# Performance work log

Measured on AMD Instinct MI355X. Metric: run time of the kernel, lower is better.

The kernel has to match this reference:

```python
import jax, jax.numpy as jnp
import numpy as np

# dims
T, B, D = 128, 512, 512          # seq, batch, d_input = dim_aug_state*n_agent
M, H, DH, DFF = 6, 2, 32, 64     # mem_len, heads, d_head_inner, d_ff_inner
ACT = 64                          # dim_action*n_agent
BG = 0.1                          # GRU-gate bias (GTrXL)


def _ln(t, g, b):
    mu = t.mean(-1, keepdims=True)
    var = ((t - mu) ** 2).mean(-1, keepdims=True)
    return (t - mu) / jnp.sqrt(var + 1e-5) * g + b


def _rel_shift(x):
    # x: [T, J, B, H] -> TransformerXL relative shift
    Tq, J = x.shape[0], x.shape[1]
    zp = jnp.zeros((Tq, 1) + x.shape[2:], x.dtype)
    x = jnp.concatenate([zp, x], axis=1)              # [T, J+1, B, H]
    x = x.reshape((J + 1, Tq) + x.shape[2:])[1:]      # [J, T, B, H]
    return x.reshape((Tq, J) + x.shape[2:])


def _gate(x, y, W, b):
    # GRU-style gating g(x, y): x = residual stream, y = new branch output
    lin = lambda t, i: t @ W[i] + b[i]
    r = jax.nn.sigmoid(lin(y, 0) + lin(x, 1))
    z = jax.nn.sigmoid(lin(y, 2) + lin(x, 3) - BG)
    h = jnp.tanh(lin(y, 4) + (r * x) @ W[5] + b[5])
    return (1.0 - z) * x + z * h


def setup_inputs() -> dict:
    key = jax.random.key(0)
    ks = iter(jax.random.split(key, 32))
    rn = lambda shape, s=0.02: jax.random.normal(next(ks), shape, jnp.float32) * s
    return dict(
        aug_states=jax.random.normal(next(ks), (T, B, D), jnp.float32),
        action=jax.random.normal(next(ks), (B, ACT), jnp.float32),
        memory=jnp.zeros((M, B, D), jnp.float32),
        W_q=rn((D, H * DH)), W_kv=rn((D, 2 * H * DH)), W_p=rn((D, H * DH)), W_out=rn((H * DH, D)),
        u=rn((H, DH)), v=rn((H, DH)),
        ln1_g=jnp.ones(D), ln1_b=jnp.zeros(D), ln2_g=jnp.ones(D), ln2_b=jnp.zeros(D),
        ff_W1=rn((D, DFF)), ff_b1=jnp.zeros(DFF), ff_W2=rn((DFF, D)), ff_b2=jnp.zeros(D),
        g1_W=rn((6, D, D)), g1_b=jnp.zeros((6, D)), g2_W=rn((6, D, D)), g2_b=jnp.zeros((6, D)),
        d1_W=rn((D, 1024)), d1_b=jnp.zeros(1024),
        d2_W=rn((1024 + ACT, 512)), d2_b=jnp.zeros(512),
        d3_W=rn((512, 300)), d3_b=jnp.zeros(300),
        d4_W=rn((300, 1)), d4_b=jnp.zeros(1),
    )


def reference(aug_states, action, memory, W_q, W_kv, W_p, W_out, u, v,
              ln1_g, ln1_b, ln2_g, ln2_b, ff_W1, ff_b1, ff_W2, ff_b2,
              g1_W, g1_b, g2_W, g2_b, d1_W, d1_b, d2_W, d2_b, d3_W, d3_b, d4_W, d4_b):
    x = aug_states                                    # [T, B, D]
    J = T + M
    # sinusoidal relative position embeddings for positions J-1 .. 0
    pos = jnp.arange(J - 1, -1, -1.0, dtype=jnp.float32)
    inv_freq = 1.0 / (10000.0 ** (jnp.arange(0, D, 2, dtype=jnp.float32) / D))
    si = pos[:, None] * inv_freq[None, :]
    pos_emb = jnp.concatenate([jnp.sin(si), jnp.cos(si)], axis=-1)   # [J, D]

    # --- stable (pre-LN + gated) TransformerXL layer ---
    src2 = _ln(x, ln1_g, ln1_b)
    cat = jnp.concatenate([memory, src2], axis=0)     # [J, B, D]
    k, vv = jnp.split(cat @ W_kv, 2, axis=-1)
    q = (src2 @ W_q).reshape(T, B, H, DH)
    k = k.reshape(J, B, H, DH)
    vv = vv.reshape(J, B, H, DH)
    p = (pos_emb @ W_p).reshape(J, H, DH)
    content = jnp.einsum("ibhd,jbhd->ijbh", q + u, k)
    position = _rel_shift(jnp.einsum("ibhd,jhd->ijbh", q + v, p))
    attn = content + position                         # [T, J, B, H]
    mask = jnp.arange(J)[None, :] > (jnp.arange(T)[:, None] + M)     # causal w/ memory offset
    attn = jnp.where(mask[:, :, None, None], -jnp.inf, attn)
    attn = jax.nn.softmax(attn * (1.0 / np.sqrt(DH)), axis=1)
    av = jnp.einsum("ijbh,jbhd->ibhd", attn, vv).reshape(T, B, H * DH)
    src = _gate(x, av @ W_out, g1_W, g1_b)
    ff = jax.nn.relu(_ln(src, ln2_g, ln2_b) @ ff_W1 + ff_b1) @ ff_W2 + ff_b2
    out = _gate(src, ff, g2_W, g2_b)                  # [T, B, D]

    # --- mean pool + MLP critic head ---
    ts = out.mean(axis=0)                             # [B, D]
    h1 = jax.nn.relu(ts @ d1_W + d1_b)
    h = jnp.concatenate([h1, action], axis=1)
    h = jax.nn.relu(h @ d2_W + d2_b)
    h = jax.nn.relu(h @ d3_W + d3_b)
    return jax.nn.relu(h @ d4_W + d4_b)               # [B, 1]
```

## Files before the change

kernel.cpp:

```cpp
#include <hip/hip_runtime.h>
#include <math.h>

namespace {

constexpr int kT = 128, kB = 512, kD = 512, kM = 6, kH = 2;
constexpr int kJ = kT + kM;
constexpr float kBG = 0.1f;
constexpr int kTB = kT * kB;
constexpr int kBK = 32;

typedef __attribute__((ext_vector_type(8))) short bf16x8;
typedef __attribute__((ext_vector_type(4))) float f32x4;
typedef __attribute__((ext_vector_type(8))) unsigned short us8;
typedef __attribute__((ext_vector_type(4))) unsigned short us4;

__device__ __forceinline__ float sigmoidf_(float x) {
  return 1.0f / (1.0f + __expf(-x));
}

__device__ __forceinline__ unsigned short bf16u(float f) {
  union { float f; unsigned u; } c; c.f = f;
  unsigned r = c.u + 0x7fffu + ((c.u >> 16) & 1u);
  return (unsigned short)(r >> 16);
}

__device__ __forceinline__ float b2f(unsigned short u) {
  union { unsigned u; float f; } c; c.u = (unsigned)u << 16;
  return c.f;
}

__device__ __forceinline__ void gl_lds16(const void* g, void* l) {
  __builtin_amdgcn_global_load_lds(
      (const __attribute__((address_space(1))) unsigned int*)g,
      (__attribute__((address_space(3))) unsigned int*)l, 16, 0, 0);
}

template <int N>
__device__ __forceinline__ void wvm_() {
  asm volatile("s_waitcnt vmcnt(%0)" :: "n"(N) : "memory");
}
__device__ __forceinline__ void bar_() { __builtin_amdgcn_s_barrier(); }
__device__ __forceinline__ void cfence_() { asm volatile("" ::: "memory"); }


__global__ __launch_bounds__(256) void transp_kernel(const float* __restrict__ W,
                                                     unsigned short* __restrict__ Wt,
                                                     int K, int N) {
  __shared__ float t[32][33];
  const int n0 = blockIdx.x * 32, k0 = blockIdx.y * 32;
  const float* Wb = W + (size_t)blockIdx.z * K * N;
  unsigned short* Wtb = Wt + (size_t)blockIdx.z * K * N;
  int tx = threadIdx.x & 31, ty = threadIdx.x >> 5;
#pragma unroll
  for (int r = 0; r < 32; r += 8)
    t[ty + r][tx] = Wb[(size_t)(k0 + ty + r) * N + n0 + tx];
  __syncthreads();
#pragma unroll
  for (int r = 0; r < 32; r += 8)
    Wtb[(size_t)(n0 + ty + r) * K + k0 + tx] = bf16u(t[tx][ty + r]);
}

__global__ __launch_bounds__(256) void conv_bf16_kernel(const float* __restrict__ in,
                                                        unsigned short* __restrict__ outb,
                                                        size_t n) {
  size_t idx = ((size_t)blockIdx.x * 256 + threadIdx.x) * 8;
  if (idx >= n) return;
  float4 a = *(const float4*)(in + idx);
  float4 c = *(const float4*)(in + idx + 4);
  us8 o;
  o[0] = bf16u(a.x); o[1] = bf16u(a.y); o[2] = bf16u(a.z); o[3] = bf16u(a.w);
  o[4] = bf16u(c.x); o[5] = bf16u(c.y); o[6] = bf16u(c.z); o[7] = bf16u(c.w);
  *(us8*)(outb + idx) = o;
}

__global__ __launch_bounds__(256) void ln1_dual_kernel(const float* __restrict__ in,
                                                       const float* __restrict__ g,
                                                       const float* __restrict__ b,
                                                       unsigned short* __restrict__ outLN,
                                                       unsigned short* __restrict__ outRaw,
                                                       int nrows) {
  int wave = threadIdx.x >> 6, lane = threadIdx.x & 63;
  int row = blockIdx.x * 4 + wave;
  if (row >= nrows) return;
  const float* p = in + (size_t)row * kD + lane * 8;
  float4 a = *(const float4*)p;
  float4 c = *(const float4*)(p + 4);
  float v[8] = {a.x, a.y, a.z, a.w, c.x, c.y, c.z, c.w};
  float s = 0.f;
#pragma unroll
  for (int i = 0; i < 8; ++i) s += v[i];
#pragma unroll
  for (int off = 32; off; off >>= 1) s += __shfl_xor(s, off);
  float mu = s * (1.0f / 512.0f);
  float q = 0.f;
#pragma unroll
  for (int i = 0; i < 8; ++i) { float d = v[i] - mu; q += d * d; }
#pragma unroll
  for (int off = 32; off; off >>= 1) q += __shfl_xor(q, off);
  float rstd = rsqrtf(q * (1.0f / 512.0f) + 1e-5f);
  us8 oln, oraw;
#pragma unroll
  for (int i = 0; i < 8; ++i) {
    int col = lane * 8 + i;
    oln[i] = bf16u((v[i] - mu) * rstd * g[col] + b[col]);
    oraw[i] = bf16u(v[i]);
  }
  size_t off8 = (size_t)row * kD + lane * 8;
  *(us8*)(outLN + off8) = oln;
  *(us8*)(outRaw + off8) = oraw;
}

__global__ __launch_bounds__(256) void ln_b16_kernel(const unsigned short* __restrict__ in,
                                                     const float* __restrict__ g,
                                                     const float* __restrict__ b,
                                                     unsigned short* __restrict__ outb,
                                                     int nrows) {
  int wave = threadIdx.x >> 6, lane = threadIdx.x & 63;
  int row = blockIdx.x * 4 + wave;
  if (row >= nrows) return;
  us8 iv = *(const us8*)(in + (size_t)row * kD + lane * 8);
  float v[8];
#pragma unroll
  for (int i = 0; i < 8; ++i) v[i] = b2f(iv[i]);
  float s = 0.f;
#pragma unroll
  for (int i = 0; i < 8; ++i) s += v[i];
#pragma unroll
  for (int off = 32; off; off >>= 1) s += __shfl_xor(s, off);
  float mu = s * (1.0f / 512.0f);
  float q = 0.f;
#pragma unroll
  for (int i = 0; i < 8; ++i) { float d = v[i] - mu; q += d * d; }
#pragma unroll
  for (int off = 32; off; off >>= 1) q += __shfl_xor(q, off);
  float rstd = rsqrtf(q * (1.0f / 512.0f) + 1e-5f);
  us8 o;
#pragma unroll
  for (int i = 0; i < 8; ++i) {
    int col = lane * 8 + i;
    o[i] = bf16u((v[i] - mu) * rstd * g[col] + b[col]);
  }
  *(us8*)(outb + (size_t)row * kD + lane * 8) = o;
}

template <int TN, int EPI>
__global__ __launch_bounds__(256) void mfma_gemm_bt(
    const unsigned short* __restrict__ A, const unsigned short* __restrict__ Bt,
    int K, const float* __restrict__ bias, void* __restrict__ Cv, int N) {
  constexpr int MI = (TN == 128) ? 4 : 2;
  constexpr int NJ = 4;
  constexpr int BCH = TN * 64 / 1024;
  constexpr int NLD = 2 + BCH / 4;
  __shared__ __align__(16) unsigned short As[3][128 * kBK];
  __shared__ __align__(16) unsigned short Bs[3][TN * kBK];
  const int tid = threadIdx.x;
  const int lane = tid & 63, wv = tid >> 6;
  const int ml = lane & 15, qd = lane >> 4;
  const int swc = ((lane & 3) ^ ((lane >> 3) & 3)) * 16;
  const int qdx = qd ^ ((ml >> 1) & 3);
  const int m0 = blockIdx.y * 128, n0 = blockIdx.x * TN;
  const int mw0 = (TN == 128) ? (wv >> 1) * 64 : wv * 32;
  const int nw0 = (TN == 128) ? (wv & 1) * 64 : 0;
  const size_t ldA = (size_t)K * 2, ldB = (size_t)K * 2;
  const char* Ab = (const char*)A + (size_t)m0 * ldA;
  const char* Bb = (const char*)Bt + (size_t)n0 * ldB;
  auto stg = [&](int k0, int buf) {
#pragma unroll
    for (int c = wv; c < 8; c += 4) {
      int fb = c * 1024 + lane * 16;
      gl_lds16(Ab + (size_t)(fb >> 6) * ldA + swc + (size_t)k0 * 2,
               (char*)As[buf] + c * 1024 + lane * 16);
    }
#pragma unroll
    for (int c = wv; c < BCH; c += 4) {
      int fb = c * 1024 + lane * 16;
      gl_lds16(Bb + (size_t)(fb >> 6) * ldB + swc + (size_t)k0 * 2,
               (char*)Bs[buf] + c * 1024 + lane * 16);
    }
  };
  f32x4 acc[MI][NJ];
#pragma unroll
  for (int i = 0; i < MI; ++i)
#pragma unroll
    for (int j = 0; j < NJ; ++j) acc[i][j] = (f32x4)0.f;
  stg(0, 0);
  stg(kBK, 1);
  int cb = 0;
  for (int k0 = 0; k0 < K; k0 += kBK) {
    const int sb = (cb == 0) ? 2 : cb - 1;
    if (k0 + 2 * kBK < K) { stg(k0 + 2 * kBK, sb); wvm_<2 * NLD>(); }
    else if (k0 + kBK < K) { wvm_<NLD>(); }
    else { wvm_<0>(); }
    bar_(); cfence_();
    bf16x8 af[MI], bfr[NJ];
#pragma unroll
    for (int i = 0; i < MI; ++i)
      af[i] = *(const bf16x8*)(As[cb] + (mw0 + i * 16 + ml) * kBK + qdx * 8);
#pragma unroll
    for (int j = 0; j < NJ; ++j)
      bfr[j] = *(const bf16x8*)(Bs[cb] + (nw0 + j * 16 + ml) * kBK + qdx * 8);
#pragma unroll
    for (int i = 0; i < MI; ++i)
#pragma unroll
      for (int j = 0; j < NJ; ++j)
        acc[i][j] = __builtin_amdgcn_mfma_f32_16x16x32_bf16(af[i], bfr[j], acc[i][j], 0, 0, 0);
    cfence_(); bar_();
    cb = (cb == 2) ? 0 : cb + 1;
  }
#pragma unroll
  for (int i = 0; i < MI; ++i)
#pragma unroll
    for (int j = 0; j < NJ; ++j)
#pragma unroll
      for (int r = 0; r < 4; ++r) {
        int m = m0 + mw0 + i * 16 + qd * 4 + r;
        int n = n0 + nw0 + j * 16 + ml;
        float val = acc[i][j][r];
        if (EPI >= 2) val += bias[n];
        if (EPI == 2) val = fmaxf(val, 0.f);
        size_t idx = (size_t)m * N + n;
        if (EPI == 0) ((float*)Cv)[idx] = val;
        else ((unsigned short*)Cv)[idx] = bf16u(val);
      }
}

template <int NBLOG>
__device__ __forceinline__ void xcd_decode(int& m0, int& n0, int tileN) {
  const int L = blockIdx.x;
  const int xcd = L & 7;
  const int s = L >> 3;
  const int mgPerX = (int)(gridDim.x >> (3 + NBLOG));
  const int mg = xcd * mgPerX + (s >> NBLOG);
  const int nb = s & ((1 << NBLOG) - 1);
  m0 = mg * 128;
  n0 = nb * tileN;
}

__global__ __launch_bounds__(512, 4) void mfma_gate_r(
    const unsigned short* __restrict__ Yb, const unsigned short* __restrict__ Xb,
    const unsigned short* __restrict__ Wt, const float* __restrict__ gb,
    unsigned short* __restrict__ RX) {
  __shared__ __align__(16) unsigned short As[3][128 * kBK];
  __shared__ __align__(16) unsigned short Bs[3][256 * kBK];
  const int tid = threadIdx.x;
  const int lane = tid & 63, wv = tid >> 6;
  const int ml = lane & 15, qd = lane >> 4;
  const int swc = ((lane & 3) ^ ((lane >> 3) & 3)) * 16;
  const int qdx = qd ^ ((ml >> 1) & 3);
  int m0, n0;
  xcd_decode<1>(m0, n0, 256);
  const int mw0 = (wv & 1) * 64, nw0 = (wv >> 1) * 64;
  const size_t ld = (size_t)kD * 2;
  const size_t DD = (size_t)kD * kD;
  const char* Abp[2], *Bbp[2];
  {
    const unsigned short* Ap[2] = {Yb, Xb};
#pragma unroll
    for (int p = 0; p < 2; ++p) {
      Abp[p] = (const char*)Ap[p] + (size_t)m0 * ld;
      Bbp[p] = (const char*)(Wt + (size_t)p * DD) + (size_t)n0 * ld;
    }
  }
  auto stg = [&](const char* Ab, const char* Bb, int k0, int buf) {
    {
      int fb = wv * 1024 + lane * 16;
      gl_lds16(Ab + (size_t)(fb >> 6) * ld + swc + (size_t)k0 * 2,
               (char*)As[buf] + fb);
    }
#pragma unroll
    for (int c = wv; c < 16; c += 8) {
      int fb = c * 1024 + lane * 16;
      gl_lds16(Bb + (size_t)(fb >> 6) * ld + swc + (size_t)k0 * 2,
               (char*)Bs[buf] + fb);
    }
  };
  f32x4 acc[4][4];
#pragma unroll
  for (int i = 0; i < 4; ++i)
#pragma unroll
    for (int j = 0; j < 4; ++j) acc[i][j] = (f32x4)0.f;
  stg(Abp[0], Bbp[0], 0, 0);
  stg(Abp[0], Bbp[0], kBK, 1);
  int cb = 0;
#pragma unroll
  for (int p = 0; p < 2; ++p) {
    for (int k = 0; k < 16; ++k) {
      const int sb = (cb == 0) ? 2 : cb - 1;
      if (k < 14) { stg(Abp[p], Bbp[p], (k + 2) * kBK, sb); wvm_<6>(); }
      else if (p < 1) { stg(Abp[p + 1], Bbp[p + 1], (k - 14) * kBK, sb); wvm_<6>(); }
      else if (k == 14) { wvm_<3>(); }
      else { wvm_<0>(); }
      bar_(); cfence_();
      bf16x8 af[4], bfr[4];
#pragma unroll
      for (int i = 0; i < 4; ++i)
        af[i] = *(const bf16x8*)(As[cb] + (mw0 + i * 16 + ml) * kBK + qdx * 8);
#pragma unroll
      for (int j = 0; j < 4; ++j)
        bfr[j] = *(const bf16x8*)(Bs[cb] + (nw0 + j * 16 + ml) * kBK + qdx * 8);
#pragma unroll
      for (int i = 0; i < 4; ++i)
#pragma unroll
        for (int j = 0; j < 4; ++j)
          acc[i][j] = __builtin_amdgcn_mfma_f32_16x16x32_bf16(af[i], bfr[j], acc[i][j], 0, 0, 0);
      cfence_(); bar_();
      cb = (cb == 2) ? 0 : cb + 1;
    }
  }
#pragma unroll
  for (int i = 0; i < 4; ++i)
#pragma unroll
    for (int j = 0; j < 4; ++j)
#pragma unroll
      for (int r = 0; r < 4; ++r) {
        int m = m0 + mw0 + i * 16 + qd * 4 + r;
        int n = n0 + nw0 + j * 16 + ml;
        float rg = sigmoidf_(acc[i][j][r] + gb[n] + gb[kD + n]);
        size_t idx = (size_t)m * kD + n;
        RX[idx] = bf16u(rg * b2f(Xb[idx]));
      }
}

template <bool POOL>
__global__ __launch_bounds__(512, 4) void mfma_gate_hz(
    const unsigned short* __restrict__ Yb, const unsigned short* __restrict__ RXb,
    const unsigned short* __restrict__ Xb, const unsigned short* __restrict__ Wt,
    const float* __restrict__ gb, unsigned short* __restrict__ OUTb,
    float* __restrict__ TS, int rowoff) {
  __shared__ __align__(16) unsigned short As[3][128 * kBK];
  __shared__ __align__(16) unsigned short Bs[3][128 * kBK];
  const int tid = threadIdx.x;
  const int lane = tid & 63, wv = tid >> 6;
  const int ml = lane & 15, qd = lane >> 4;
  const int swc = ((lane & 3) ^ ((lane >> 3) & 3)) * 16;
  const int qdx = qd ^ ((ml >> 1) & 3);
  int m0, n0;
  xcd_decode<2>(m0, n0, 128);
  const int mw0 = (wv & 3) * 32, nw0 = (wv >> 2) * 64;
  const size_t ld = (size_t)kD * 2;
  const size_t DD = (size_t)kD * kD;
  f32x4 accH[2][4], accZ[2][4];
#pragma unroll
  for (int i = 0; i < 2; ++i)
#pragma unroll
    for (int j = 0; j < 4; ++j) { accH[i][j] = (f32x4)0.f; accZ[i][j] = (f32x4)0.f; }
  const char* Abp[4], *Bbp[4];
  {
    const unsigned short* Ap[4] = {Yb, RXb, Yb, Xb};
    const int wsel[4] = {4, 5, 2, 3};
#pragma unroll
    for (int p = 0; p < 4; ++p) {
      Abp[p] = (const char*)Ap[p] + (size_t)m0 * ld;
      Bbp[p] = (const char*)(Wt + (size_t)wsel[p] * DD) + (size_t)n0 * ld;
    }
  }
  auto stg = [&](const char* Ab, const char* Bb, int k0, int buf) {
    int fb = wv * 1024 + lane * 16;
    size_t go = (size_t)(fb >> 6) * ld + swc + (size_t)k0 * 2;
    gl_lds16(Ab + go, (char*)As[buf] + fb);
    gl_lds16(Bb + go, (char*)Bs[buf] + fb);
  };
  stg(Abp[0], Bbp[0], 0, 0);
  stg(Abp[0], Bbp[0], kBK, 1);
  int cb = 0;
#pragma unroll
  for (int p = 0; p < 4; ++p) {
    f32x4 (*acc)[4] = (p < 2) ? accH : accZ;
    for (int k = 0; k < 16; ++k) {
      const int sb = (cb == 0) ? 2 : cb - 1;
      if (k < 14) { stg(Abp[p], Bbp[p], (k + 2) * kBK, sb); wvm_<4>(); }
      else if (p < 3) { stg(Abp[p + 1], Bbp[p + 1], (k - 14) * kBK, sb); wvm_<4>(); }
      else if (k == 14) { wvm_<2>(); }
      else { wvm_<0>(); }
      bar_(); cfence_();
      bf16x8 af[2], bfr[4];
#pragma unroll
      for (int i = 0; i < 2; ++i)
        af[i] = *(const bf16x8*)(As[cb] + (mw0 + i * 16 + ml) * kBK + qdx * 8);
#pragma unroll
      for (int j = 0; j < 4; ++j)
        bfr[j] = *(const bf16x8*)(Bs[cb] + (nw0 + j * 16 + ml) * kBK + qdx * 8);
#pragma unroll
      for (int i = 0; i < 2; ++i)
#pragma unroll
        for (int j = 0; j < 4; ++j)
          acc[i][j] = __builtin_amdgcn_mfma_f32_16x16x32_bf16(af[i], bfr[j], acc[i][j], 0, 0, 0);
      cfence_(); bar_();
      cb = (cb == 2) ? 0 : cb + 1;
    }
  }
#pragma unroll
  for (int i = 0; i < 2; ++i)
#pragma unroll
    for (int j = 0; j < 4; ++j)
#pragma unroll
      for (int r = 0; r < 4; ++r) {
        int m = m0 + mw0 + i * 16 + qd * 4 + r;
        int n = n0 + nw0 + j * 16 + ml;
        float z = sigmoidf_(accZ[i][j][r] + gb[2 * kD + n] + gb[3 * kD + n] - kBG);
        float hc = tanhf(accH[i][j][r] + gb[4 * kD + n] + gb[5 * kD + n]);
        size_t idx = (size_t)m * kD + n;
        float val = (1.0f - z) * b2f(Xb[idx]) + z * hc;
        if (POOL) {
          int b = (rowoff + m) & (kB - 1);
          atomicAdd(TS + (size_t)b * kD + n, val * (1.0f / kT));
        } else {
          OUTb[idx] = bf16u(val);
        }
      }
}

__global__ __launch_bounds__(64) void posp_kernel(const float* __restrict__ Wp,
                                                  float* __restrict__ P) {
  __shared__ float emb[512];
  int jj = blockIdx.x;
  int t = threadIdx.x;
  float pos = (float)(kJ - 1 - jj);
#pragma unroll
  for (int r = 0; r < 8; ++r) {
    int d = t + r * 64;
    int i = (d < 256) ? d : d - 256;
    float invf = expf(-((float)(2 * i) * (1.0f / 512.0f)) * 9.210340371976184f);
    float si = pos * invf;
    emb[d] = (d < 256) ? sinf(si) : cosf(si);
  }
  __syncthreads();
  float acc = 0.f;
  for (int d = 0; d < 512; ++d) acc = fmaf(emb[d], Wp[d * 64 + t], acc);
  P[jj * 64 + t] = acc;
}

__global__ __launch_bounds__(128) void attn_kernel(
    const float* __restrict__ Q, const unsigned short* __restrict__ KV,
    const float* __restrict__ P, const float* __restrict__ U,
    const float* __restrict__ V, unsigned short* __restrict__ AV) {
  __shared__ float ks[kJ][32];
  __shared__ float vs[kJ][32];
  __shared__ float ps[32][kJ + 2];
  const int b = blockIdx.x, h = blockIdx.y;
  const int tid = threadIdx.x;
  for (int idx = tid; idx < kJ * 8; idx += 128) {
    int j = idx >> 3, seg = idx & 7;
    const unsigned short* src = KV + ((size_t)(j * kB + b)) * 128 + h * 32 + seg * 4;
    us4 kq = *(const us4*)src;
    us4 vq = *(const us4*)(src + 64);
#pragma unroll
    for (int e = 0; e < 4; ++e) {
      ks[j][seg * 4 + e] = b2f(kq[e]);
      vs[j][seg * 4 + e] = b2f(vq[e]);
    }
  }
  for (int idx = tid; idx < kJ * 8; idx += 128) {
    int j = idx >> 3, seg = idx & 7;
    float4 pq = *(const float4*)(P + j * 64 + h * 32 + seg * 4);
    ps[seg * 4 + 0][j] = pq.x;
    ps[seg * 4 + 1][j] = pq.y;
    ps[seg * 4 + 2][j] = pq.z;
    ps[seg * 4 + 3][j] = pq.w;
  }
  __syncthreads();
  const int i = tid;
  float qu[32], qv[32];
  const float* qp = Q + ((size_t)(i * kB + b)) * 64 + h * 32;
#pragma unroll
  for (int d = 0; d < 32; ++d) {
    float qd = qp[d];
    qu[d] = qd + U[h * 32 + d];
    qv[d] = qd + V[h * 32 + d];
  }
  float m = -INFINITY, l = 0.f, acc[32] = {};
  const float scale = 0.17677669529663687f;
  for (int j = 0; j <= i + kM; ++j) {
    float s = 0.f;
#pragma unroll
    for (int d = 0; d < 32; d += 4) {
      float4 k4 = *(const float4*)&ks[j][d];
      s = fmaf(qu[d + 0], k4.x, s);
      s = fmaf(qu[d + 1], k4.y, s);
      s = fmaf(qu[d + 2], k4.z, s);
      s = fmaf(qu[d + 3], k4.w, s);
    }
    int jj = j + (kT - 1) - i;
#pragma unroll
    for (int d = 0; d < 32; ++d) s = fmaf(qv[d], ps[d][jj], s);
    float ls = s * scale;
    float nm = fmaxf(m, ls);
    float w = __expf(ls - nm);
    float f = __expf(m - nm);
    l = l * f + w;
#pragma unroll
    for (int d = 0; d < 32; d += 4) {
      float4 v4 = *(const float4*)&vs[j][d];
      acc[d + 0] = fmaf(acc[d + 0], f, w * v4.x);
      acc[d + 1] = fmaf(acc[d + 1], f, w * v4.y);
      acc[d + 2] = fmaf(acc[d + 2], f, w * v4.z);
      acc[d + 3] = fmaf(acc[d + 3], f, w * v4.w);
    }
    m = nm;
  }
  float inv = 1.0f / l;
  unsigned short* o = AV + ((size_t)(i * kB + b)) * 64 + h * 32;
#pragma unroll
  for (int d = 0; d < 32; ++d) o[d] = bf16u(acc[d] * inv);
}

template <int ACTF, bool DUAL>
__global__ __launch_bounds__(256) void gemm_kernel(
    const float* __restrict__ A1, const float* __restrict__ Bm1, int K1,
    const float* __restrict__ A2, const float* __restrict__ Bm2, int K2,
    const float* __restrict__ bias, float* __restrict__ C, int Mrows, int N) {
  __shared__ float As[16][68];
  __shared__ float Bs[16][68];
  const int tid = threadIdx.x;
  const int tx = tid & 15, ty = tid >> 4;
  const int m0 = blockIdx.y * 64, n0 = blockIdx.x * 64;
  const int ar = tid >> 2, aseg = tid & 3;
  float acc[4][4] = {};
#pragma unroll
  for (int pass = 0; pass < (DUAL ? 2 : 1); ++pass) {
    const float* A = (DUAL && pass) ? A2 : A1;
    const float* Bm = (DUAL && pass) ? Bm2 : Bm1;
    const int K = (DUAL && pass) ? K2 : K1;
    for (int k0 = 0; k0 < K; k0 += 16) {
      {
        int row = m0 + ar;
        int kb = k0 + aseg * 4;
        float x0 = 0.f, x1 = 0.f, x2 = 0.f, x3 = 0.f;
        if (row < Mrows) {
          const float* ap = A + (size_t)row * K + kb;
          if (kb + 3 < K) {
            float4 t = *(const float4*)ap;
            x0 = t.x; x1 = t.y; x2 = t.z; x3 = t.w;
          } else {
            if (kb + 0 < K) x0 = ap[0];
            if (kb + 1 < K) x1 = ap[1];
            if (kb + 2 < K) x2 = ap[2];
          }
        }
        As[aseg * 4 + 0][ar] = x0;
        As[aseg * 4 + 1][ar] = x1;
        As[aseg * 4 + 2][ar] = x2;
        As[aseg * 4 + 3][ar] = x3;
      }
      {
        int krow = k0 + ty;
        int nb = n0 + tx * 4;
        float y0 = 0.f, y1 = 0.f, y2 = 0.f, y3 = 0.f;
        if (krow < K) {
          const float* bp = Bm + (size_t)krow * N + nb;
          if (nb + 3 < N) {
            float4 t = *(const float4*)bp;
            y0 = t.x; y1 = t.y; y2 = t.z; y3 = t.w;
          } else {
            if (nb + 0 < N) y0 = bp[0];
            if (nb + 1 < N) y1 = bp[1];
            if (nb + 2 < N) y2 = bp[2];
          }
        }
        *(float4*)&Bs[ty][tx * 4] = make_float4(y0, y1, y2, y3);
      }
      __syncthreads();
#pragma unroll
      for (int kk = 0; kk < 16; ++kk) {
        float a[4], bb[4];
        *(float4*)a = *(const float4*)&As[kk][ty * 4];
        *(float4*)bb = *(const float4*)&Bs[kk][tx * 4];
#pragma unroll
        for (int i = 0; i < 4; ++i)
#pragma unroll
          for (int j = 0; j < 4; ++j) acc[i][j] = fmaf(a[i], bb[j], acc[i][j]);
      }
      __syncthreads();
    }
  }
#pragma unroll
  for (int i = 0; i < 4; ++i) {
    int m = m0 + ty * 4 + i;
    if (m >= Mrows) continue;
#pragma unroll
    for (int j = 0; j < 4; ++j) {
      int n = n0 + tx * 4 + j;
      if (n >= N) continue;
      float val = acc[i][j];
      if (bias) val += bias[n];
      if (ACTF == 1) val = fmaxf(val, 0.f);
      C[(size_t)m * N + n] = val;
    }
  }
}

}

extern "C" void kernel_launch(void* const* d_in, const int* in_sizes, int n_in,
                              void* d_out, int out_size, void* d_ws, size_t ws_size,
                              hipStream_t stream) {
  (void)in_sizes; (void)n_in; (void)out_size;
  const float* aug    = (const float*)d_in[0];
  const float* action = (const float*)d_in[1];
  const float* memory = (const float*)d_in[2];
  const float* W_q    = (const float*)d_in[3];
  const float* W_kv   = (const float*)d_in[4];
  const float* W_p    = (const float*)d_in[5];
  const float* W_out  = (const float*)d_in[6];
  const float* u      = (const float*)d_in[7];
  const float* v      = (const float*)d_in[8];
  const float* ln1_g  = (const float*)d_in[9];
  const float* ln1_b  = (const float*)d_in[10];
  const float* ln2_g  = (const float*)d_in[11];
  const float* ln2_b  = (const float*)d_in[12];
  const float* ff_W1  = (const float*)d_in[13];
  const float* ff_b1  = (const float*)d_in[14];
  const float* ff_W2  = (const float*)d_in[15];
  const float* ff_b2  = (const float*)d_in[16];
  const float* g1_W   = (const float*)d_in[17];
  const float* g1_b   = (const float*)d_in[18];
  const float* g2_W   = (const float*)d_in[19];
  const float* g2_b   = (const float*)d_in[20];
  const float* d1_W   = (const float*)d_in[21];
  const float* d1_b   = (const float*)d_in[22];
  const float* d2_W   = (const float*)d_in[23];
  const float* d2_b   = (const float*)d_in[24];
  const float* d3_W   = (const float*)d_in[25];
  const float* d3_b   = (const float*)d_in[26];
  const float* d4_W   = (const float*)d_in[27];
  const float* d4_b   = (const float*)d_in[28];
  float* out = (float*)d_out;

  char* base = (char*)d_ws;
  auto alloc = [&](size_t bytes) -> char* {
    char* p = base;
    base += (bytes + 255) & ~(size_t)255;
    return p;
  };
  unsigned short* Wqt  = (unsigned short*)alloc((size_t)64 * 512 * 2);
  unsigned short* Wkvt = (unsigned short*)alloc((size_t)128 * 512 * 2);
  unsigned short* Wot  = (unsigned short*)alloc((size_t)512 * 64 * 2);
  unsigned short* Wf1t = (unsigned short*)alloc((size_t)64 * 512 * 2);
  unsigned short* Wf2t = (unsigned short*)alloc((size_t)512 * 64 * 2);
  unsigned short* G1t  = (unsigned short*)alloc((size_t)6 * 512 * 512 * 2);
  unsigned short* G2t  = (unsigned short*)alloc((size_t)6 * 512 * 512 * 2);
  unsigned short* Memb = (unsigned short*)alloc((size_t)3072 * 512 * 2);
  unsigned short* KVb  = (unsigned short*)alloc((size_t)kJ * kB * 128 * 2);
  float* Qb  = (float*)alloc((size_t)kTB * 64 * 4);
  unsigned short* AVb = (unsigned short*)alloc((size_t)kTB * 64 * 2);
  unsigned short* Xb  = (unsigned short*)alloc((size_t)kTB * kD * 2);
  float* Pb  = (float*)alloc((size_t)kJ * 64 * 4);
  float* TSb = (float*)alloc((size_t)kB * kD * 4);
  float* H1b = (float*)alloc((size_t)kB * 1024 * 4);
  float* H2b = (float*)alloc((size_t)kB * 512 * 4);
  float* H3b = (float*)alloc((size_t)kB * 320 * 4);
  size_t fixedBytes = (size_t)(base - (char*)d_ws);
  const size_t ln1Bytes = (size_t)kTB * kD * 2;
  int nch = 1;
  while (nch < 32) {
    size_t chunkBytes = (size_t)(kTB / nch) * 4224 + 4096;
    size_t reuse = chunkBytes > ln1Bytes ? chunkBytes : ln1Bytes;
    if (fixedBytes + reuse <= ws_size) break;
    nch <<= 1;
  }
  const int CR = kTB / nch;
  char* R = base;
  unsigned short* L1b = (unsigned short*)R;
  char* rp = R;
  auto ralloc = [&](size_t bytes) -> char* {
    char* p = rp;
    rp += (bytes + 255) & ~(size_t)255;
    return p;
  };
  unsigned short* Ycb   = (unsigned short*)ralloc((size_t)CR * 512 * 2);
  unsigned short* RXcb  = (unsigned short*)ralloc((size_t)CR * 512 * 2);
  unsigned short* SRCcb = (unsigned short*)ralloc((size_t)CR * 512 * 2);
  unsigned short* LN2cb = (unsigned short*)ralloc((size_t)CR * 512 * 2);
  unsigned short* F1cb  = (unsigned short*)ralloc((size_t)CR * 64 * 2);

  const float* np = nullptr;
  const int MG = CR / 128;

  hipMemsetAsync(TSb, 0, (size_t)kB * kD * sizeof(float), stream);
  transp_kernel<<<dim3(2, 16, 1), 256, 0, stream>>>(W_q, Wqt, 512, 64);
  transp_kernel<<<dim3(4, 16, 1), 256, 0, stream>>>(W_kv, Wkvt, 512, 128);
  transp_kernel<<<dim3(16, 2, 1), 256, 0, stream>>>(W_out, Wot, 64, 512);
  transp_kernel<<<dim3(2, 16, 1), 256, 0, stream>>>(ff_W1, Wf1t, 512, 64);
  transp_kernel<<<dim3(16, 2, 1), 256, 0, stream>>>(ff_W2, Wf2t, 64, 512);
  transp_kernel<<<dim3(16, 16, 6), 256, 0, stream>>>(g1_W, G1t, 512, 512);
  transp_kernel<<<dim3(16, 16, 6), 256, 0, stream>>>(g2_W, G2t, 512, 512);
  conv_bf16_kernel<<<(3072 * 512 / 8 + 255) / 256, 256, 0, stream>>>(
      memory, Memb, (size_t)3072 * 512);
  ln1_dual_kernel<<<kTB / 4, 256, 0, stream>>>(aug, ln1_g, ln1_b, L1b, Xb, kTB);
  mfma_gemm_bt<128, 1><<<dim3(1, 3072 / 128), 256, 0, stream>>>(
      Memb, Wkvt, 512, np, KVb, 128);
  mfma_gemm_bt<128, 1><<<dim3(1, kTB / 128), 256, 0, stream>>>(
      L1b, Wkvt, 512, np, KVb + (size_t)3072 * 128, 128);
  mfma_gemm_bt<64, 0><<<dim3(1, kTB / 128), 256, 0, stream>>>(
      L1b, Wqt, 512, np, Qb, 64);
  posp_kernel<<<kJ, 64, 0, stream>>>(W_p, Pb);
  attn_kernel<<<dim3(kB, kH), 128, 0, stream>>>(Qb, KVb, Pb, u, v, AVb);

  for (int c = 0; c < nch; ++c) {
    const int R0 = c * CR;
    const unsigned short* Xc = Xb + (size_t)R0 * kD;
    mfma_gemm_bt<128, 1><<<dim3(4, MG), 256, 0, stream>>>(
        AVb + (size_t)R0 * 64, Wot, 64, np, Ycb, 512);
    mfma_gate_r<<<2 * MG, 512, 0, stream>>>(Ycb, Xc, G1t, g1_b, RXcb);
    mfma_gate_hz<false><<<4 * MG, 512, 0, stream>>>(
        Ycb, RXcb, Xc, G1t, g1_b, SRCcb, nullptr, R0);
    ln_b16_kernel<<<CR / 4, 256, 0, stream>>>(SRCcb, ln2_g, ln2_b, LN2cb, CR);
    mfma_gemm_bt<64, 2><<<dim3(1, MG), 256, 0, stream>>>(
        LN2cb, Wf1t, 512, ff_b1, F1cb, 64);
    mfma_gemm_bt<128, 3><<<dim3(4, MG), 256, 0, stream>>>(
        F1cb, Wf2t, 64, ff_b2, Ycb, 512);
    mfma_gate_r<<<2 * MG, 512, 0, stream>>>(Ycb, SRCcb, G2t, g2_b, RXcb);
    mfma_gate_hz<true><<<4 * MG, 512, 0, stream>>>(
        Ycb, RXcb, SRCcb, G2t, g2_b, nullptr, TSb, R0);
  }

  gemm_kernel<1, false><<<dim3(16, kB / 64), 256, 0, stream>>>(
      TSb, d1_W, 512, np, np, 0, d1_b, H1b, kB, 1024);
  gemm_kernel<1, true><<<dim3(8, kB / 64), 256, 0, stream>>>(
      H1b, d2_W, 1024, action, d2_W + (size_t)1024 * 512, 64, d2_b, H2b, kB, 512);
  gemm_kernel<1, false><<<dim3(5, kB / 64), 256, 0, stream>>>(
      H2b, d3_W, 512, np, np, 0, d3_b, H3b, kB, 300);
  gemm_kernel<1, false><<<dim3(1, kB / 64), 256, 0, stream>>>(
      H3b, d4_W, 300, np, np, 0, d4_b, out, kB, 1);
}
```

Before: 1.490 ms.

## Compute z gate alongside r gate; leave only h GEMM in second gate kernel

The GRU gate work is rebalanced. The first kernel now computes both the r and z gates, with the grid doubled and split by N-half. The z gate is stored as a 16-bit fixed-point value in a reused buffer, and the second kernel computes only the h path with wider 128x256 tiles. This evens the GEMM work between the two launches and uses larger tiles for the h GEMM, at the cost of an extra write and read of z per element and a quantisation change for z.

```diff
diff --git a/kernel.cpp b/kernel.cpp
--- a/kernel.cpp
+++ b/kernel.cpp
@@ -236,10 +236,113 @@
   n0 = nb * tileN;
 }
 
-__global__ __launch_bounds__(512, 4) void mfma_gate_r(
+__global__ __launch_bounds__(512, 4) void mfma_gate_rz(
     const unsigned short* __restrict__ Yb, const unsigned short* __restrict__ Xb,
     const unsigned short* __restrict__ Wt, const float* __restrict__ gb,
-    unsigned short* __restrict__ RX) {
+    unsigned short* __restrict__ RX, unsigned short* __restrict__ Zq) {
+  __shared__ __align__(16) unsigned short As[3][128 * kBK];
+  __shared__ __align__(16) unsigned short Bs[3][256 * kBK];
+  const int tid = threadIdx.x;
+  const int lane = tid & 63, wv = tid >> 6;
+  const int ml = lane & 15, qd = lane >> 4;
+  const int swc = ((lane & 3) ^ ((lane >> 3) & 3)) * 16;
+  const int qdx = qd ^ ((ml >> 1) & 3);
+  int m0, n0;
+  xcd_decode<2>(m0, n0, 256);
+  const int nhalf = n0 >> 9;
+  const int n0e = n0 & 511;
+  const int mw0 = (wv & 1) * 64, nw0 = (wv >> 1) * 64;
+  const size_t ld = (size_t)kD * 2;
+  const size_t DD = (size_t)kD * kD;
+  const char* Abp[2], *Bbp[2];
+  {
+    const unsigned short* Ap[2] = {Yb, Xb};
+#pragma unroll
+    for (int p = 0; p < 2; ++p) {
+      Abp[p] = (const char*)Ap[p] + (size_t)m0 * ld;
+      Bbp[p] = (const char*)(Wt + (size_t)(2 * nhalf + p) * DD) + (size_t)n0e * ld;
+    }
+  }
+  auto stg = [&](const char* Ab, const char* Bb, int k0, int buf) {
+    {
+      int fb = wv * 1024 + lane * 16;
+      gl_lds16(Ab + (size_t)(fb >> 6) * ld + swc + (size_t)k0 * 2,
+               (char*)As[buf] + fb);
+    }
+#pragma unroll
+    for (int c = wv; c < 16; c += 8) {
+      int fb = c * 1024 + lane * 16;
+      gl_lds16(Bb + (size_t)(fb >> 6) * ld + swc + (size_t)k0 * 2,
+               (char*)Bs[buf] + fb);
+    }
+  };
+  f32x4 acc[4][4];
+#pragma unroll
+  for (int i = 0; i < 4; ++i)
+#pragma unroll
+    for (int j = 0; j < 4; ++j) acc[i][j] = (f32x4)0.f;
+  stg(Abp[0], Bbp[0], 0, 0);
+  stg(Abp[0], Bbp[0], kBK, 1);
+  int cb = 0;
+#pragma unroll
+  for (int p = 0; p < 2; ++p) {
+    for (int k = 0; k < 16; ++k) {
+      const int sb = (cb == 0) ? 2 : cb - 1;
+      if (k < 14) { stg(Abp[p], Bbp[p], (k + 2) * kBK, sb); wvm_<6>(); }
+      else if (p < 1) { stg(Abp[p + 1], Bbp[p + 1], (k - 14) * kBK, sb); wvm_<6>(); }
+      else if (k == 14) { wvm_<3>(); }
+      else { wvm_<0>(); }
+      bar_(); cfence_();
+      bf16x8 af[4], bfr[4];
+#pragma unroll
+      for (int i = 0; i < 4; ++i)
+        af[i] = *(const bf16x8*)(As[cb] + (mw0 + i * 16 + ml) * kBK + qdx * 8);
+#pragma unroll
+      for (int j = 0; j < 4; ++j)
+        bfr[j] = *(const bf16x8*)(Bs[cb] + (nw0 + j * 16 + ml) * kBK + qdx * 8);
+#pragma unroll
+      for (int i = 0; i < 4; ++i)
+#pragma unroll
+        for (int j = 0; j < 4; ++j)
+          acc[i][j] = __builtin_amdgcn_mfma_f32_16x16x32_bf16(af[i], bfr[j], acc[i][j], 0, 0, 0);
+      cfence_(); bar_();
+      cb = (cb == 2) ? 0 : cb + 1;
+    }
+  }
+  if (nhalf == 0) {
+#pragma unroll
+    for (int i = 0; i < 4; ++i)
+#pragma unroll
+      for (int j = 0; j < 4; ++j)
+#pragma unroll
+        for (int r = 0; r < 4; ++r) {
+          int m = m0 + mw0 + i * 16 + qd * 4 + r;
+          int n = n0e + nw0 + j * 16 + ml;
+          float rg = sigmoidf_(acc[i][j][r] + gb[n] + gb[kD + n]);
+          size_t idx = (size_t)m * kD + n;
+          RX[idx] = bf16u(rg * b2f(Xb[idx]));
+        }
+  } else {
+#pragma unroll
+    for (int i = 0; i < 4; ++i)
+#pragma unroll
+      for (int j = 0; j < 4; ++j)
+#pragma unroll
+        for (int r = 0; r < 4; ++r) {
+          int m = m0 + mw0 + i * 16 + qd * 4 + r;
+          int n = n0e + nw0 + j * 16 + ml;
+          float z = sigmoidf_(acc[i][j][r] + gb[2 * kD + n] + gb[3 * kD + n] - kBG);
+          Zq[(size_t)m * kD + n] = (unsigned short)(z * 65535.f + 0.5f);
+        }
+  }
+}
+
+template <bool POOL>
+__global__ __launch_bounds__(512, 4) void mfma_gate_h(
+    const unsigned short* __restrict__ Yb, const unsigned short* __restrict__ RXb,
+    const unsigned short* __restrict__ Xb, const unsigned short* __restrict__ Wt,
+    const float* __restrict__ gb, const unsigned short* __restrict__ Zq,
+    unsigned short* __restrict__ OUTb, float* __restrict__ TS, int rowoff) {
   __shared__ __align__(16) unsigned short As[3][128 * kBK];
   __shared__ __align__(16) unsigned short Bs[3][256 * kBK];
   const int tid = threadIdx.x;
@@ -254,11 +357,11 @@
   const size_t DD = (size_t)kD * kD;
   const char* Abp[2], *Bbp[2];
   {
-    const unsigned short* Ap[2] = {Yb, Xb};
+    const unsigned short* Ap[2] = {Yb, RXb};
 #pragma unroll
     for (int p = 0; p < 2; ++p) {
       Abp[p] = (const char*)Ap[p] + (size_t)m0 * ld;
-      Bbp[p] = (const char*)(Wt + (size_t)p * DD) + (size_t)n0 * ld;
+      Bbp[p] = (const char*)(Wt + (size_t)(4 + p) * DD) + (size_t)n0 * ld;
     }
   }
   auto stg = [&](const char* Ab, const char* Bb, int k0, int buf) {
@@ -315,91 +418,9 @@
       for (int r = 0; r < 4; ++r) {
         int m = m0 + mw0 + i * 16 + qd * 4 + r;
         int n = n0 + nw0 + j * 16 + ml;
-        float rg = sigmoidf_(acc[i][j][r] + gb[n] + gb[kD + n]);
         size_t idx = (size_t)m * kD + n;
-        RX[idx] = bf16u(rg * b2f(Xb[idx]));
-      }
-}
-
-template <bool POOL>
-__global__ __launch_bounds__(512, 4) void mfma_gate_hz(
-    const unsigned short* __restrict__ Yb, const unsigned short* __restrict__ RXb,
-    const unsigned short* __restrict__ Xb, const unsigned short* __restrict__ Wt,
-    const float* __restrict__ gb, unsigned short* __restrict__ OUTb,
-    float* __restrict__ TS, int rowoff) {
-  __shared__ __align__(16) unsigned short As[3][128 * kBK];
-  __shared__ __align__(16) unsigned short Bs[3][128 * kBK];
-  const int tid = threadIdx.x;
-  const int lane = tid & 63, wv = tid >> 6;
-  const int ml = lane & 15, qd = lane >> 4;
-  const int swc = ((lane & 3) ^ ((lane >> 3) & 3)) * 16;
-  const int qdx = qd ^ ((ml >> 1) & 3);
-  int m0, n0;
-  xcd_decode<2>(m0, n0, 128);
-  const int mw0 = (wv & 3) * 32, nw0 = (wv >> 2) * 64;
-  const size_t ld = (size_t)kD * 2;
-  const size_t DD = (size_t)kD * kD;
-  f32x4 accH[2][4], accZ[2][4];
-#pragma unroll
-  for (int i = 0; i < 2; ++i)
-#pragma unroll
-    for (int j = 0; j < 4; ++j) { accH[i][j] = (f32x4)0.f; accZ[i][j] = (f32x4)0.f; }
-  const char* Abp[4], *Bbp[4];
-  {
-    const unsigned short* Ap[4] = {Yb, RXb, Yb, Xb};
-    const int wsel[4] = {4, 5, 2, 3};
-#pragma unroll
-    for (int p = 0; p < 4; ++p) {
-      Abp[p] = (const char*)Ap[p] + (size_t)m0 * ld;
-      Bbp[p] = (const char*)(Wt + (size_t)wsel[p] * DD) + (size_t)n0 * ld;
-    }
-  }
-  auto stg = [&](const char* Ab, const char* Bb, int k0, int buf) {
-    int fb = wv * 1024 + lane * 16;
-    size_t go = (size_t)(fb >> 6) * ld + swc + (size_t)k0 * 2;
-    gl_lds16(Ab + go, (char*)As[buf] + fb);
-    gl_lds16(Bb + go, (char*)Bs[buf] + fb);
-  };
-  stg(Abp[0], Bbp[0], 0, 0);
-  stg(Abp[0], Bbp[0], kBK, 1);
-  int cb = 0;
-#pragma unroll
-  for (int p = 0; p < 4; ++p) {
-    f32x4 (*acc)[4] = (p < 2) ? accH : accZ;
-    for (int k = 0; k < 16; ++k) {
-      const int sb = (cb == 0) ? 2 : cb - 1;
-      if (k < 14) { stg(Abp[p], Bbp[p], (k + 2) * kBK, sb); wvm_<4>(); }
-      else if (p < 3) { stg(Abp[p + 1], Bbp[p + 1], (k - 14) * kBK, sb); wvm_<4>(); }
-      else if (k == 14) { wvm_<2>(); }
-      else { wvm_<0>(); }
-      bar_(); cfence_();
-      bf16x8 af[2], bfr[4];
-#pragma unroll
-      for (int i = 0; i < 2; ++i)
-        af[i] = *(const bf16x8*)(As[cb] + (mw0 + i * 16 + ml) * kBK + qdx * 8);
-#pragma unroll
-      for (int j = 0; j < 4; ++j)
-        bfr[j] = *(const bf16x8*)(Bs[cb] + (nw0 + j * 16 + ml) * kBK + qdx * 8);
-#pragma unroll
-      for (int i = 0; i < 2; ++i)
-#pragma unroll
-        for (int j = 0; j < 4; ++j)
-          acc[i][j] = __builtin_amdgcn_mfma_f32_16x16x32_bf16(af[i], bfr[j], acc[i][j], 0, 0, 0);
-      cfence_(); bar_();
-      cb = (cb == 2) ? 0 : cb + 1;
-    }
-  }
-#pragma unroll
-  for (int i = 0; i < 2; ++i)
-#pragma unroll
-    for (int j = 0; j < 4; ++j)
-#pragma unroll
-      for (int r = 0; r < 4; ++r) {
-        int m = m0 + mw0 + i * 16 + qd * 4 + r;
-        int n = n0 + nw0 + j * 16 + ml;
-        float z = sigmoidf_(accZ[i][j][r] + gb[2 * kD + n] + gb[3 * kD + n] - kBG);
-        float hc = tanhf(accH[i][j][r] + gb[4 * kD + n] + gb[5 * kD + n]);
-        size_t idx = (size_t)m * kD + n;
+        float z = (float)Zq[idx] * (1.0f / 65535.0f);
+        float hc = tanhf(acc[i][j][r] + gb[4 * kD + n] + gb[5 * kD + n]);
         float val = (1.0f - z) * b2f(Xb[idx]) + z * hc;
         if (POOL) {
           int b = (rowoff + m) & (kB - 1);
@@ -672,6 +693,7 @@
   unsigned short* SRCcb = (unsigned short*)ralloc((size_t)CR * 512 * 2);
   unsigned short* LN2cb = (unsigned short*)ralloc((size_t)CR * 512 * 2);
   unsigned short* F1cb  = (unsigned short*)ralloc((size_t)CR * 64 * 2);
+  unsigned short* Zqb = LN2cb;
 
   const float* np = nullptr;
   const int MG = CR / 128;
@@ -701,17 +723,17 @@
     const unsigned short* Xc = Xb + (size_t)R0 * kD;
     mfma_gemm_bt<128, 1><<<dim3(4, MG), 256, 0, stream>>>(
         AVb + (size_t)R0 * 64, Wot, 64, np, Ycb, 512);
-    mfma_gate_r<<<2 * MG, 512, 0, stream>>>(Ycb, Xc, G1t, g1_b, RXcb);
-    mfma_gate_hz<false><<<4 * MG, 512, 0, stream>>>(
-        Ycb, RXcb, Xc, G1t, g1_b, SRCcb, nullptr, R0);
+    mfma_gate_rz<<<4 * MG, 512, 0, stream>>>(Ycb, Xc, G1t, g1_b, RXcb, Zqb);
+    mfma_gate_h<false><<<2 * MG, 512, 0, stream>>>(
+        Ycb, RXcb, Xc, G1t, g1_b, Zqb, SRCcb, nullptr, R0);
     ln_b16_kernel<<<CR / 4, 256, 0, stream>>>(SRCcb, ln2_g, ln2_b, LN2cb, CR);
     mfma_gemm_bt<64, 2><<<dim3(1, MG), 256, 0, stream>>>(
         LN2cb, Wf1t, 512, ff_b1, F1cb, 64);
     mfma_gemm_bt<128, 3><<<dim3(4, MG), 256, 0, stream>>>(
         F1cb, Wf2t, 64, ff_b2, Ycb, 512);
-    mfma_gate_r<<<2 * MG, 512, 0, stream>>>(Ycb, SRCcb, G2t, g2_b, RXcb);
-    mfma_gate_hz<true><<<4 * MG, 512, 0, stream>>>(
-        Ycb, RXcb, SRCcb, G2t, g2_b, nullptr, TSb, R0);
+    mfma_gate_rz<<<4 * MG, 512, 0, stream>>>(Ycb, SRCcb, G2t, g2_b, RXcb, Zqb);
+    mfma_gate_h<true><<<2 * MG, 512, 0, stream>>>(
+        Ycb, RXcb, SRCcb, G2t, g2_b, Zqb, nullptr, TSb, R0);
   }
 
   gemm_kernel<1, false><<<dim3(16, kB / 64), 256, 0, stream>>>(
```

New measurement: 1.524 ms. 2.3% more time.
